# Performance work log

Hardware: AMD Instinct MI355X
Metric: run time of the kernel (lower is better)

Reference implementation:

```python
import jax, jax.numpy as jnp
import numpy as np

LN_EPS = 1e-5

def _layer_norm(x, gamma, beta):
    mu = jnp.mean(x, axis=-1, keepdims=True)
    var = jnp.mean(jnp.square(x - mu), axis=-1, keepdims=True)
    return (x - mu) * jax.lax.rsqrt(var + LN_EPS) * gamma + beta

def setup_inputs() -> dict:
    key = jax.random.key(0)
    ks = jax.random.split(key, 10)
    B, S, D_IN = 8, 2048, 1024
    H1, H2, C = 2048, 1024, 64
    s1 = 1.0 / np.sqrt(D_IN)
    s2 = 1.0 / np.sqrt(H1)
    s3 = 1.0 / np.sqrt(H2)
    return {
        "embeddings": jax.random.normal(ks[0], (B, S, D_IN), jnp.float32),
        "prior_evidence": jax.random.normal(ks[1], (B, C), jnp.float32),
        "W1": jax.random.uniform(ks[2], (D_IN, H1), jnp.float32, -s1, s1),
        "b1": jnp.zeros((H1,), jnp.float32),
        "g1": jnp.ones((H1,), jnp.float32),
        "beta1": jnp.zeros((H1,), jnp.float32),
        "W2": jax.random.uniform(ks[3], (H1, H2), jnp.float32, -s2, s2),
        "b2": jnp.zeros((H2,), jnp.float32),
        "g2": jnp.ones((H2,), jnp.float32),
        "beta2": jnp.zeros((H2,), jnp.float32),
        "Wh": jax.random.uniform(ks[4], (H2, C), jnp.float32, -s3, s3),
        "bh": jnp.zeros((C,), jnp.float32),
        "and_gate": jnp.ones((C,), jnp.float32),
        "or_gate": jnp.ones((C,), jnp.float32),
    }

def reference(embeddings, prior_evidence, W1, b1, g1, beta1, W2, b2, g2, beta2, Wh, bh, and_gate, or_gate):
    # feature extractor: Linear -> ReLU -> Dropout(eval: identity) -> LayerNorm, x2
    h = _layer_norm(jax.nn.relu(embeddings @ W1 + b1), g1, beta1)
    features = _layer_norm(jax.nn.relu(h @ W2 + b2), g2, beta2)  # [B,S,H2]
    d = features.shape[-1]
    scores = jnp.einsum('bsd,btd->bst', features, features) / jnp.sqrt(jnp.float32(d))
    attention_weights = jax.nn.softmax(scores, axis=-1)          # [B,S,S]
    attended = jnp.einsum('bst,btd->bsd', attention_weights, features)
    logits = attended @ Wh + bh                                   # [B,S,C]
    sig_l = jax.nn.sigmoid(logits)
    sig_p = jax.nn.sigmoid(prior_evidence)[:, None, :]            # [B,1,C] broadcasts
    and_ev = jnp.minimum(sig_l, sig_p) * and_gate
    or_ev = jnp.maximum(sig_l, sig_p) * or_gate
    logits = jnp.log((and_ev + or_ev) / 2 + 1e-10)
    return (logits, attention_weights)
```

## Files before the change

### kernel.cpp

```cpp
#include <hip/hip_runtime.h>

typedef unsigned short u16;
typedef __bf16 bf16x8 __attribute__((ext_vector_type(8)));
typedef float f32x4 __attribute__((ext_vector_type(4)));

__device__ __forceinline__ u16 f2bf(float f) {
    unsigned u = __float_as_uint(f);
    u = (u + 0x7FFFu + ((u >> 16) & 1u)) >> 16;
    return (u16)u;
}
__device__ __forceinline__ float bf2f(u16 h) {
    return __uint_as_float(((unsigned)h) << 16);
}

__device__ __forceinline__ void gld16(const u16* g, u16* l) {
    __builtin_amdgcn_global_load_lds((const __attribute__((address_space(1))) void*)g,
                                     (__attribute__((address_space(3))) void*)l, 16, 0, 0);
}

__global__ __launch_bounds__(256) void cvt_kernel(const float* __restrict__ in,
                                                  u16* __restrict__ out, long n) {
    long i = ((long)blockIdx.x * blockDim.x + threadIdx.x) * 4;
    if (i + 3 < n) {
        float4 v = *(const float4*)&in[i];
        __align__(8) u16 r[4] = {f2bf(v.x), f2bf(v.y), f2bf(v.z), f2bf(v.w)};
        *(int2*)&out[i] = *(const int2*)r;
    }
}

template <int INF32>
__global__ __launch_bounds__(256) void transpose_to_bf16(const void* __restrict__ in,
                                                         u16* __restrict__ out, int R, int C,
                                                         long inB, long outB) {
    __shared__ float tile[32][33];
    const long zi = (long)blockIdx.z * inB;
    const long zo = (long)blockIdx.z * outB;
    const int c0 = blockIdx.x * 32, r0 = blockIdx.y * 32;
    const int tx = threadIdx.x & 31;
    const int ty = threadIdx.x >> 5;
#pragma unroll
    for (int i = 0; i < 32; i += 8) {
        long idx = zi + (long)(r0 + ty + i) * C + c0 + tx;
        float v = INF32 ? ((const float*)in)[idx] : bf2f(((const u16*)in)[idx]);
        tile[ty + i][tx] = v;
    }
    __syncthreads();
#pragma unroll
    for (int i = 0; i < 32; i += 8) {
        out[zo + (long)(c0 + ty + i) * R + r0 + tx] = f2bf(tile[tx][ty + i]);
    }
}

template <int OUTBF>
__global__ __launch_bounds__(256, 3) void gemm_nt(const u16* __restrict__ A,
                                                  const u16* __restrict__ Bm,
                                                  void* __restrict__ Cout, int M, int N, int K,
                                                  long sA, long sB, long sC,
                                                  const float* __restrict__ bias, int act,
                                                  float scale, int symm,
                                                  const float* __restrict__ rscale) {
    int bx, by, zz;
    if (symm) {
        const int q = gridDim.x >> 3;
        const int orig = blockIdx.x;
        const int wgid = (orig & 7) * q + (orig >> 3);
        const int NB = N >> 7;
        const int nTri = (NB * (NB + 1)) >> 1;
        zz = wgid / nTri;
        int t = wgid - zz * nTri;
        by = 0;
        int rem = NB;
        while (t >= rem) {
            t -= rem;
            --rem;
            ++by;
        }
        bx = by + t;
    } else {
        const int nx = gridDim.x;
        const int nwg = nx * gridDim.y;
        const int orig = blockIdx.y * nx + blockIdx.x;
        const int q = nwg >> 3, r = nwg & 7, xcd = orig & 7, o8 = orig >> 3;
        const int wgid = (xcd < r ? xcd * (q + 1) : r * (q + 1) + (xcd - r) * q) + o8;
        bx = wgid % nx;
        by = wgid / nx;
        zz = blockIdx.z;
    }

    __shared__ __align__(16) u16 As[2][128 * 32];
    __shared__ __align__(16) u16 Bs[2][128 * 32];
    const int tid = threadIdx.x;
    const int lane = tid & 63;
    const int wid = tid >> 6;
    const int wr = wid >> 1;
    const int wc = wid & 1;
    const int l15 = lane & 15, lg = lane >> 4;
    const long zA = (long)zz * sA;
    const long zB = (long)zz * sB;
    const long zC = (long)zz * sC;
    const int m0 = by * 128, n0 = bx * 128;
    const u16* Ab = A + zA + (long)m0 * K;
    const u16* Bb = Bm + zB + (long)n0 * K;
    const int nt = K >> 5;

    f32x4 acc[4][4] = {};

    auto stage = [&](int x, int b) {
#pragma unroll
        for (int j = 0; j < 2; ++j) {
            const int c = j * 256 + tid;
            const int row = c >> 2;
            const int col = (((c & 3) ^ ((row >> 1) & 3)) << 3);
            gld16(Ab + (long)row * K + x * 32 + col, &As[b][c * 8]);
            gld16(Bb + (long)row * K + x * 32 + col, &Bs[b][c * 8]);
        }
    };

    stage(0, 0);
    asm volatile("s_waitcnt vmcnt(0)" ::: "memory");
    __builtin_amdgcn_s_barrier();

    const int sx = (l15 >> 1) & 3;
    const int go = ((lg ^ sx) << 3) + (l15 & 1) * 0;

    for (int t = 0; t < nt; ++t) {
        const int cur = t & 1;
        if (t + 1 < nt) stage(t + 1, cur ^ 1);
        bf16x8 af[4], bf[4];
#pragma unroll
        for (int n = 0; n < 4; ++n)
            bf[n] = *(const bf16x8*)&Bs[cur][(wc * 64 + n * 16 + l15) * 32 + go];
#pragma unroll
        for (int m = 0; m < 4; ++m)
            af[m] = *(const bf16x8*)&As[cur][(wr * 64 + m * 16 + l15) * 32 + go];
        __builtin_amdgcn_s_setprio(1);
#pragma unroll
        for (int m = 0; m < 4; ++m)
#pragma unroll
            for (int n = 0; n < 4; ++n)
                acc[m][n] =
                    __builtin_amdgcn_mfma_f32_16x16x32_bf16(af[m], bf[n], acc[m][n], 0, 0, 0);
        __builtin_amdgcn_s_setprio(0);
        asm volatile("s_waitcnt vmcnt(0)" ::: "memory");
        __builtin_amdgcn_s_barrier();
    }

#pragma unroll
    for (int n = 0; n < 4; ++n) {
        const int col = n0 + wc * 64 + n * 16 + l15;
        const float bv = bias ? bias[col] : 0.0f;
#pragma unroll
        for (int m = 0; m < 4; ++m) {
            const int rowb = m0 + wr * 64 + m * 16 + lg * 4;
            float v[4];
#pragma unroll
            for (int r = 0; r < 4; ++r) {
                float f = acc[m][n][r] * scale + bv;
                if (act == 1)
                    f = fmaxf(f, 0.0f);
                else if (act == 2)
                    f = __expf(f - 32.0f);
                if (rscale) f *= rscale[(long)zz * M + rowb + r];
                v[r] = f;
                if (OUTBF)
                    ((u16*)Cout)[zC + (long)(rowb + r) * N + col] = f2bf(f);
                else
                    ((float*)Cout)[zC + (long)(rowb + r) * N + col] = f;
            }
            if (symm && bx > by) {
                if (OUTBF) {
                    __align__(8) u16 tv[4] = {f2bf(v[0]), f2bf(v[1]), f2bf(v[2]), f2bf(v[3])};
                    *(int2*)&((u16*)Cout)[zC + (long)col * N + rowb] = *(const int2*)tv;
                } else {
                    *(float4*)&((float*)Cout)[zC + (long)col * N + rowb] =
                        make_float4(v[0], v[1], v[2], v[3]);
                }
            }
        }
    }
}

template <int CH>
__global__ __launch_bounds__(256) void ln_wave(u16* __restrict__ x, const float* __restrict__ g,
                                               const float* __restrict__ be) {
    const int lane = threadIdx.x & 63;
    const int wid = threadIdx.x >> 6;
    const long row = (long)blockIdx.x * 4 + wid;
    u16* p = x + row * (CH * 512);
    __align__(16) u16 raw[CH][8];
    float s = 0.f, ss = 0.f;
#pragma unroll
    for (int c = 0; c < CH; ++c) {
        *(int4*)raw[c] = *(const int4*)&p[(c * 64 + lane) * 8];
#pragma unroll
        for (int j = 0; j < 8; ++j) {
            float f = bf2f(raw[c][j]);
            s += f;
            ss += f * f;
        }
    }
#pragma unroll
    for (int o = 1; o < 64; o <<= 1) {
        s += __shfl_xor(s, o);
        ss += __shfl_xor(ss, o);
    }
    const float inv = 1.0f / (float)(CH * 512);
    const float mu = s * inv;
    const float var = ss * inv - mu * mu;
    const float rs = rsqrtf(var + 1e-5f);
#pragma unroll
    for (int c = 0; c < CH; ++c) {
        const int base = (c * 64 + lane) * 8;
        float4 g0 = *(const float4*)&g[base];
        float4 g1 = *(const float4*)&g[base + 4];
        float4 b0 = *(const float4*)&be[base];
        float4 b1 = *(const float4*)&be[base + 4];
        float gv[8] = {g0.x, g0.y, g0.z, g0.w, g1.x, g1.y, g1.z, g1.w};
        float bv[8] = {b0.x, b0.y, b0.z, b0.w, b1.x, b1.y, b1.z, b1.w};
#pragma unroll
        for (int j = 0; j < 8; ++j)
            raw[c][j] = f2bf((bf2f(raw[c][j]) - mu) * rs * gv[j] + bv[j]);
        *(int4*)&p[base] = *(const int4*)raw[c];
    }
}

__global__ __launch_bounds__(256) void norm_wave(const u16* __restrict__ e,
                                                 float* __restrict__ outw,
                                                 float* __restrict__ rowInv) {
    const int lane = threadIdx.x & 63;
    const int wid = threadIdx.x >> 6;
    const long row = (long)blockIdx.x * 4 + wid;
    const u16* p = e + row * 2048;
    float v[4][8];
    float s = 0.f;
#pragma unroll
    for (int c = 0; c < 4; ++c) {
        __align__(16) u16 raw[8];
        *(int4*)raw = *(const int4*)&p[(c * 64 + lane) * 8];
#pragma unroll
        for (int j = 0; j < 8; ++j) {
            v[c][j] = bf2f(raw[j]);
            s += v[c][j];
        }
    }
#pragma unroll
    for (int o = 1; o < 64; o <<= 1) s += __shfl_xor(s, o);
    const float inv = 1.0f / s;
    if (lane == 0) rowInv[row] = inv;
    float* q = outw + row * 2048;
#pragma unroll
    for (int c = 0; c < 4; ++c) {
        const int base = (c * 64 + lane) * 8;
        float4 o0 = make_float4(v[c][0] * inv, v[c][1] * inv, v[c][2] * inv, v[c][3] * inv);
        float4 o1 = make_float4(v[c][4] * inv, v[c][5] * inv, v[c][6] * inv, v[c][7] * inv);
        *(float4*)&q[base] = o0;
        *(float4*)&q[base + 4] = o1;
    }
}

__global__ __launch_bounds__(256) void head_kernel(const u16* __restrict__ A,
                                                   const u16* __restrict__ WhT,
                                                   const float* __restrict__ bh,
                                                   const float* __restrict__ prior,
                                                   const float* __restrict__ ag,
                                                   const float* __restrict__ og,
                                                   float* __restrict__ out) {
    __shared__ __align__(16) u16 As2[128 * 64];
    __shared__ __align__(16) u16 Bs2[64 * 64];
    const int tid = threadIdx.x;
    const int lane = tid & 63;
    const int wid = tid >> 6;
    const int l15 = lane & 15, lg = lane >> 4;
    const int m0 = blockIdx.x * 128;
    const int srow = tid >> 3, scol = (tid & 7) * 8;
    const u16* pa = A + (long)(m0 + srow) * 1024 + scol;
    const u16* pb = WhT + (long)srow * 1024 + scol;

    f32x4 acc[2][4] = {};
    for (int k0 = 0; k0 < 1024; k0 += 64) {
#pragma unroll
        for (int i = 0; i < 4; ++i) gld16(pa + (long)i * 32 * 1024 + k0, &As2[i * 2048 + tid * 8]);
#pragma unroll
        for (int i = 0; i < 2; ++i) gld16(pb + (long)i * 32 * 1024 + k0, &Bs2[i * 2048 + tid * 8]);
        __syncthreads();
#pragma unroll
        for (int kk = 0; kk < 2; ++kk) {
            bf16x8 af[2], bfr[4];
#pragma unroll
            for (int m = 0; m < 2; ++m)
                af[m] = *(const bf16x8*)&As2[(wid * 32 + m * 16 + l15) * 64 + kk * 32 + lg * 8];
#pragma unroll
            for (int n = 0; n < 4; ++n)
                bfr[n] = *(const bf16x8*)&Bs2[(n * 16 + l15) * 64 + kk * 32 + lg * 8];
#pragma unroll
            for (int m = 0; m < 2; ++m)
#pragma unroll
                for (int n = 0; n < 4; ++n)
                    acc[m][n] =
                        __builtin_amdgcn_mfma_f32_16x16x32_bf16(af[m], bfr[n], acc[m][n], 0, 0, 0);
        }
        __syncthreads();
    }

#pragma unroll
    for (int n = 0; n < 4; ++n) {
        const int col = n * 16 + l15;
        const float bhv = bh[col];
        const float agv = ag[col];
        const float ogv = og[col];
#pragma unroll
        for (int m = 0; m < 2; ++m) {
#pragma unroll
            for (int r = 0; r < 4; ++r) {
                const int row = m0 + wid * 32 + m * 16 + lg * 4 + r;
                const float logit = acc[m][n][r] + bhv;
                const int b = row >> 11;
                const float sp = 1.f / (1.f + expf(-prior[b * 64 + col]));
                const float sl = 1.f / (1.f + expf(-logit));
                const float av = fminf(sl, sp) * agv;
                const float ov = fmaxf(sl, sp) * ogv;
                out[(long)row * 64 + col] = logf((av + ov) * 0.5f + 1e-10f);
            }
        }
    }
}

extern "C" void kernel_launch(void* const* d_in, const int* in_sizes, int n_in, void* d_out,
                              int out_size, void* d_ws, size_t ws_size, hipStream_t stream) {
    const float* emb = (const float*)d_in[0];
    const float* prior = (const float*)d_in[1];
    const float* W1 = (const float*)d_in[2];
    const float* b1 = (const float*)d_in[3];
    const float* g1 = (const float*)d_in[4];
    const float* be1 = (const float*)d_in[5];
    const float* W2 = (const float*)d_in[6];
    const float* b2 = (const float*)d_in[7];
    const float* g2 = (const float*)d_in[8];
    const float* be2 = (const float*)d_in[9];
    const float* Wh = (const float*)d_in[10];
    const float* bh = (const float*)d_in[11];
    const float* ag = (const float*)d_in[12];
    const float* og = (const float*)d_in[13];

    const int Bn = 8, S = 2048, DIN = 1024, H1 = 2048, H2 = 1024, Cc = 64;
    const int M = Bn * S;

    char* ws = (char*)d_ws;
    size_t off = 0;
    auto alloc = [&](size_t b) {
        size_t o = off;
        off += (b + 255) & ~(size_t)255;
        return o;
    };
    char* R0 = ws + alloc((size_t)M * H1 * 2);
    char* R1 = ws + alloc((size_t)M * DIN * 2);
    char* R2 = ws + alloc((size_t)M * H2 * 2);
    u16* W1t = (u16*)(ws + alloc((size_t)H1 * DIN * 2));
    u16* W2t = (u16*)(ws + alloc((size_t)H2 * H1 * 2));
    u16* WhT = (u16*)(ws + alloc((size_t)Cc * H2 * 2));
    float* rowInv = (float*)(ws + alloc((size_t)M * 4));

    u16* h = (u16*)R0;
    u16* attnb = (u16*)R0;
    u16* embb = (u16*)R1;
    u16* featT = (u16*)R1;
    u16* feat = (u16*)R2;
    u16* attd = (u16*)R2;

    float* out_logits = (float*)d_out;
    float* out_attn = out_logits + (size_t)M * Cc;

    cvt_kernel<<<(int)(((long)M * DIN) / 1024), 256, 0, stream>>>(emb, embb, (long)M * DIN);
    transpose_to_bf16<1><<<dim3(H1 / 32, DIN / 32, 1), 256, 0, stream>>>(W1, W1t, DIN, H1, 0, 0);
    transpose_to_bf16<1><<<dim3(H2 / 32, H1 / 32, 1), 256, 0, stream>>>(W2, W2t, H1, H2, 0, 0);
    transpose_to_bf16<1><<<dim3(Cc / 32, H2 / 32, 1), 256, 0, stream>>>(Wh, WhT, H2, Cc, 0, 0);
    gemm_nt<1><<<dim3(H1 / 128, M / 128, 1), 256, 0, stream>>>(embb, W1t, h, M, H1, DIN, 0, 0, 0,
                                                               b1, 1, 1.0f, 0, nullptr);
    ln_wave<4><<<M / 4, 256, 0, stream>>>(h, g1, be1);
    gemm_nt<1><<<dim3(H2 / 128, M / 128, 1), 256, 0, stream>>>(h, W2t, feat, M, H2, H1, 0, 0, 0,
                                                               b2, 1, 1.0f, 0, nullptr);
    ln_wave<2><<<M / 4, 256, 0, stream>>>(feat, g2, be2);
    transpose_to_bf16<0><<<dim3(H2 / 32, S / 32, Bn), 256, 0, stream>>>(
        feat, featT, S, H2, (long)S * H2, (long)H2 * S);
    {
        const int NB = S / 128;
        const int nTri = NB * (NB + 1) / 2;
        gemm_nt<1><<<dim3(nTri * Bn, 1, 1), 256, 0, stream>>>(
            feat, feat, attnb, S, S, H2, (long)S * H2, (long)S * H2, (long)S * S, nullptr,
            2, 0.03125f, 1, nullptr);
    }
    norm_wave<<<M / 4, 256, 0, stream>>>(attnb, out_attn, rowInv);
    gemm_nt<1><<<dim3(H2 / 128, S / 128, Bn), 256, 0, stream>>>(attnb, featT, attd, S, H2, S,
                                                                (long)S * S, (long)H2 * S,
                                                                (long)S * H2, nullptr, 0, 1.0f, 0,
                                                                rowInv);
    head_kernel<<<M / 128, 256, 0, stream>>>(attd, WhT, bh, prior, ag, og, out_logits);
}
```

Before: 481.1 us.

## Enlarge GEMM tiles to 256x256 with 8 waves and 4-stage LDS pipeline

The bf16 GEMM kernel moves from 128x128 tiles with 4 waves and double buffering to 256x256 tiles with 8 waves, each wave computing 128x64 in two halves. Global-to-LDS loads become a 4-deep ring, three tiles ahead, with partial vmcnt waits and extra barriers interleaved between the MFMA halves. The aim is more operand reuse per loaded byte and better hiding of load latency. In exchange it uses 128KB of LDS per block and more accumulator registers, so occupancy drops, and the grids get fewer, larger blocks, which can hurt tail balance on the smaller GEMMs.

```diff
diff --git a/kernel.cpp b/kernel.cpp
--- a/kernel.cpp
+++ b/kernel.cpp
@@ -52,7 +52,7 @@
 }
 
 template <int OUTBF>
-__global__ __launch_bounds__(256, 3) void gemm_nt(const u16* __restrict__ A,
+__global__ __launch_bounds__(512, 2) void gemm_nt(const u16* __restrict__ A,
                                                   const u16* __restrict__ Bm,
                                                   void* __restrict__ Cout, int M, int N, int K,
                                                   long sA, long sB, long sC,
@@ -64,7 +64,7 @@
         const int q = gridDim.x >> 3;
         const int orig = blockIdx.x;
         const int wgid = (orig & 7) * q + (orig >> 3);
-        const int NB = N >> 7;
+        const int NB = N >> 8;
         const int nTri = (NB * (NB + 1)) >> 1;
         zz = wgid / nTri;
         int t = wgid - zz * nTri;
@@ -87,52 +87,58 @@
         zz = blockIdx.z;
     }
 
-    __shared__ __align__(16) u16 As[2][128 * 32];
-    __shared__ __align__(16) u16 Bs[2][128 * 32];
+    __shared__ __align__(16) u16 As[4][256 * 32];
+    __shared__ __align__(16) u16 Bs[4][256 * 32];
     const int tid = threadIdx.x;
     const int lane = tid & 63;
     const int wid = tid >> 6;
-    const int wr = wid >> 1;
-    const int wc = wid & 1;
+    const int wr = wid >> 2;
+    const int wc = wid & 3;
     const int l15 = lane & 15, lg = lane >> 4;
     const long zA = (long)zz * sA;
     const long zB = (long)zz * sB;
     const long zC = (long)zz * sC;
-    const int m0 = by * 128, n0 = bx * 128;
+    const int m0 = by * 256, n0 = bx * 256;
     const u16* Ab = A + zA + (long)m0 * K;
     const u16* Bb = Bm + zB + (long)n0 * K;
     const int nt = K >> 5;
 
-    f32x4 acc[4][4] = {};
-
-    auto stage = [&](int x, int b) {
-#pragma unroll
-        for (int j = 0; j < 2; ++j) {
-            const int c = j * 256 + tid;
-            const int row = c >> 2;
-            const int col = (((c & 3) ^ ((row >> 1) & 3)) << 3);
-            gld16(Ab + (long)row * K + x * 32 + col, &As[b][c * 8]);
-            gld16(Bb + (long)row * K + x * 32 + col, &Bs[b][c * 8]);
-        }
+    f32x4 acc[8][4] = {};
+
+    auto stage_chunk = [&](int x, int j) {
+        const int b = x & 3;
+        const int c = j * 512 + tid;
+        const int row = c >> 2;
+        const int col = (((c & 3) ^ ((row >> 1) & 3)) << 3);
+        gld16(Ab + (long)row * K + x * 32 + col, &As[b][c * 8]);
+        gld16(Bb + (long)row * K + x * 32 + col, &Bs[b][c * 8]);
     };
 
-    stage(0, 0);
-    asm volatile("s_waitcnt vmcnt(0)" ::: "memory");
+#pragma unroll
+    for (int x = 0; x < 3; ++x) {
+        stage_chunk(x, 0);
+        stage_chunk(x, 1);
+    }
+    asm volatile("s_waitcnt vmcnt(8)" ::: "memory");
     __builtin_amdgcn_s_barrier();
 
     const int sx = (l15 >> 1) & 3;
-    const int go = ((lg ^ sx) << 3) + (l15 & 1) * 0;
+    const int go = ((lg ^ sx) << 3);
 
     for (int t = 0; t < nt; ++t) {
-        const int cur = t & 1;
-        if (t + 1 < nt) stage(t + 1, cur ^ 1);
-        bf16x8 af[4], bf[4];
+        const u16* Ac = &As[t & 3][0];
+        const u16* Bc = &Bs[t & 3][0];
+        bf16x8 bf[4], af[4];
 #pragma unroll
         for (int n = 0; n < 4; ++n)
-            bf[n] = *(const bf16x8*)&Bs[cur][(wc * 64 + n * 16 + l15) * 32 + go];
+            bf[n] = *(const bf16x8*)&Bc[(wc * 64 + n * 16 + l15) * 32 + go];
 #pragma unroll
         for (int m = 0; m < 4; ++m)
-            af[m] = *(const bf16x8*)&As[cur][(wr * 64 + m * 16 + l15) * 32 + go];
+            af[m] = *(const bf16x8*)&Ac[(wr * 128 + m * 16 + l15) * 32 + go];
+        if (t + 3 < nt) stage_chunk(t + 3, 0);
+        __builtin_amdgcn_s_barrier();
+        asm volatile("s_waitcnt lgkmcnt(0)" ::: "memory");
+        __builtin_amdgcn_sched_barrier(0);
         __builtin_amdgcn_s_setprio(1);
 #pragma unroll
         for (int m = 0; m < 4; ++m)
@@ -141,7 +147,29 @@
                 acc[m][n] =
                     __builtin_amdgcn_mfma_f32_16x16x32_bf16(af[m], bf[n], acc[m][n], 0, 0, 0);
         __builtin_amdgcn_s_setprio(0);
-        asm volatile("s_waitcnt vmcnt(0)" ::: "memory");
+        __builtin_amdgcn_s_barrier();
+#pragma unroll
+        for (int m = 0; m < 4; ++m)
+            af[m] = *(const bf16x8*)&Ac[(wr * 128 + 64 + m * 16 + l15) * 32 + go];
+        if (t + 3 < nt) stage_chunk(t + 3, 1);
+        __builtin_amdgcn_s_barrier();
+        asm volatile("s_waitcnt lgkmcnt(0)" ::: "memory");
+        __builtin_amdgcn_sched_barrier(0);
+        __builtin_amdgcn_s_setprio(1);
+#pragma unroll
+        for (int m = 0; m < 4; ++m)
+#pragma unroll
+            for (int n = 0; n < 4; ++n)
+                acc[4 + m][n] = __builtin_amdgcn_mfma_f32_16x16x32_bf16(af[m], bf[n],
+                                                                        acc[4 + m][n], 0, 0, 0);
+        __builtin_amdgcn_s_setprio(0);
+        if (t + 3 < nt) {
+            asm volatile("s_waitcnt vmcnt(8)" ::: "memory");
+        } else if (t + 2 < nt) {
+            asm volatile("s_waitcnt vmcnt(4)" ::: "memory");
+        } else if (t + 1 < nt) {
+            asm volatile("s_waitcnt vmcnt(0)" ::: "memory");
+        }
         __builtin_amdgcn_s_barrier();
     }
 
@@ -150,8 +178,8 @@
         const int col = n0 + wc * 64 + n * 16 + l15;
         const float bv = bias ? bias[col] : 0.0f;
 #pragma unroll
-        for (int m = 0; m < 4; ++m) {
-            const int rowb = m0 + wr * 64 + m * 16 + lg * 4;
+        for (int m = 0; m < 8; ++m) {
+            const int rowb = m0 + wr * 128 + m * 16 + lg * 4;
             float v[4];
 #pragma unroll
             for (int r = 0; r < 4; ++r) {
@@ -374,23 +402,23 @@
     transpose_to_bf16<1><<<dim3(H1 / 32, DIN / 32, 1), 256, 0, stream>>>(W1, W1t, DIN, H1, 0, 0);
     transpose_to_bf16<1><<<dim3(H2 / 32, H1 / 32, 1), 256, 0, stream>>>(W2, W2t, H1, H2, 0, 0);
     transpose_to_bf16<1><<<dim3(Cc / 32, H2 / 32, 1), 256, 0, stream>>>(Wh, WhT, H2, Cc, 0, 0);
-    gemm_nt<1><<<dim3(H1 / 128, M / 128, 1), 256, 0, stream>>>(embb, W1t, h, M, H1, DIN, 0, 0, 0,
+    gemm_nt<1><<<dim3(H1 / 256, M / 256, 1), 512, 0, stream>>>(embb, W1t, h, M, H1, DIN, 0, 0, 0,
                                                                b1, 1, 1.0f, 0, nullptr);
     ln_wave<4><<<M / 4, 256, 0, stream>>>(h, g1, be1);
-    gemm_nt<1><<<dim3(H2 / 128, M / 128, 1), 256, 0, stream>>>(h, W2t, feat, M, H2, H1, 0, 0, 0,
+    gemm_nt<1><<<dim3(H2 / 256, M / 256, 1), 512, 0, stream>>>(h, W2t, feat, M, H2, H1, 0, 0, 0,
                                                                b2, 1, 1.0f, 0, nullptr);
     ln_wave<2><<<M / 4, 256, 0, stream>>>(feat, g2, be2);
     transpose_to_bf16<0><<<dim3(H2 / 32, S / 32, Bn), 256, 0, stream>>>(
         feat, featT, S, H2, (long)S * H2, (long)H2 * S);
     {
-        const int NB = S / 128;
+        const int NB = S / 256;
         const int nTri = NB * (NB + 1) / 2;
-        gemm_nt<1><<<dim3(nTri * Bn, 1, 1), 256, 0, stream>>>(
+        gemm_nt<1><<<dim3(nTri * Bn, 1, 1), 512, 0, stream>>>(
             feat, feat, attnb, S, S, H2, (long)S * H2, (long)S * H2, (long)S * S, nullptr,
             2, 0.03125f, 1, nullptr);
     }
     norm_wave<<<M / 4, 256, 0, stream>>>(attnb, out_attn, rowInv);
-    gemm_nt<1><<<dim3(H2 / 128, S / 128, Bn), 256, 0, stream>>>(attnb, featT, attd, S, H2, S,
+    gemm_nt<1><<<dim3(H2 / 256, S / 256, Bn), 512, 0, stream>>>(attnb, featT, attd, S, H2, S,
                                                                 (long)S * S, (long)H2 * S,
                                                                 (long)S * H2, nullptr, 0, 1.0f, 0,
                                                                 rowInv);
```

New measurement: 480.0 us. No clear change (-0.2%).
